# Kernel tuning notes

Hardware: AMD Instinct MI355X
Metric: run time of the kernel (lower is better)

## Reference

```python
import jax, jax.numpy as jnp
import numpy as np

REG_MAX = 16
NUM_CLASSES = 80
STRIDES = (32, 16, 8)
HWS = [(20, 20), (40, 40), (80, 80)]
OFFSET = 0.5


def _conv(x, w, b=None, pad=0):
    out = jax.lax.conv_general_dilated(x, w, (1, 1), [(pad, pad), (pad, pad)],
                                       dimension_numbers=('NCHW', 'OIHW', 'NCHW'))
    if b is not None:
        out = out + b[None, :, None, None]
    return out


def _swish(x):
    return x * jax.nn.sigmoid(x)


def _ese(feat, avg, fc_w, fc_b, conv_w, bn_s, bn_b):
    # ESEAttn: sigmoid-gated 1x1 conv + BN(affine, eval) + swish
    gate = jax.nn.sigmoid(_conv(avg, fc_w, fc_b))
    x = _conv(feat * gate, conv_w)
    return _swish(x * bn_s[None, :, None, None] + bn_b[None, :, None, None])


def _head_scale(feat, ps, proj):
    (cfw, cfb, ccw, cbs, cbb, rfw, rfb, rcw, rbs, rbb, pcw, pcb, prw, prb) = ps
    b, c, h, w = feat.shape
    l = h * w
    avg = jnp.mean(feat, axis=(2, 3), keepdims=True)  # adaptive_avg_pool2d to 1x1
    cls_logit = _conv(_ese(feat, avg, cfw, cfb, ccw, cbs, cbb) + feat, pcw, pcb, pad=1)
    cls_score = jax.nn.sigmoid(cls_logit).reshape(b, NUM_CLASSES, l)
    reg = _conv(_ese(feat, avg, rfw, rfb, rcw, rbs, rbb), prw, prb, pad=1)
    reg = reg.reshape(b, 4, REG_MAX + 1, l).transpose(0, 2, 1, 3)  # [b, reg_max+1, 4, l]
    reg = jax.nn.softmax(reg, axis=1)
    reg_dist = jnp.einsum('r,brfl->bfl', proj, reg)  # DFL integral (proj_conv)
    return cls_score, reg_dist


def _anchors():
    pts, st = [], []
    for (h, w), s in zip(HWS, STRIDES):
        sx = jnp.arange(w, dtype=jnp.float32) + OFFSET
        sy = jnp.arange(h, dtype=jnp.float32) + OFFSET
        yy, xx = jnp.meshgrid(sy, sx, indexing='ij')
        pts.append(jnp.stack([xx, yy], -1).reshape(-1, 2))
        st.append(jnp.full((h * w, 1), s, dtype=jnp.float32))
    return jnp.concatenate(pts, 0), jnp.concatenate(st, 0)


def setup_inputs() -> dict:
    key = jax.random.key(0)
    chans = [1024, 512, 256]
    B = 16
    keys = iter(jax.random.split(key, 128))
    inp = {}
    for i, (c, (h, w)) in enumerate(zip(chans, HWS)):
        s = 1.0 / np.sqrt(c)
        inp[f'feat{i}'] = jax.random.normal(next(keys), (B, c, h, w), jnp.float32)
        for br in ('cls', 'reg'):
            inp[f'p{i}_{br}_fc_w'] = jax.random.normal(next(keys), (c, c, 1, 1), jnp.float32) * 0.001
            inp[f'p{i}_{br}_fc_b'] = jnp.zeros((c,), jnp.float32)
            inp[f'p{i}_{br}_conv_w'] = jax.random.normal(next(keys), (c, c, 1, 1), jnp.float32) * s
            inp[f'p{i}_{br}_bn_s'] = 1.0 + 0.1 * jax.random.normal(next(keys), (c,), jnp.float32)
            inp[f'p{i}_{br}_bn_b'] = 0.1 * jax.random.normal(next(keys), (c,), jnp.float32)
        inp[f'p{i}_cls_pred_w'] = jax.random.normal(next(keys), (NUM_CLASSES, c, 3, 3), jnp.float32) * s * 0.1
        inp[f'p{i}_cls_pred_b'] = jnp.full((NUM_CLASSES,), -4.595, jnp.float32)  # bias_init_with_prob(0.01)
        inp[f'p{i}_reg_pred_w'] = jax.random.normal(next(keys), (4 * (REG_MAX + 1), c, 3, 3), jnp.float32) * s * 0.1
        inp[f'p{i}_reg_pred_b'] = jnp.ones((4 * (REG_MAX + 1),), jnp.float32)
    return inp


def reference(feat0, feat1, feat2,
              p0_cls_fc_w, p0_cls_fc_b, p0_cls_conv_w, p0_cls_bn_s, p0_cls_bn_b,
              p0_reg_fc_w, p0_reg_fc_b, p0_reg_conv_w, p0_reg_bn_s, p0_reg_bn_b,
              p0_cls_pred_w, p0_cls_pred_b, p0_reg_pred_w, p0_reg_pred_b,
              p1_cls_fc_w, p1_cls_fc_b, p1_cls_conv_w, p1_cls_bn_s, p1_cls_bn_b,
              p1_reg_fc_w, p1_reg_fc_b, p1_reg_conv_w, p1_reg_bn_s, p1_reg_bn_b,
              p1_cls_pred_w, p1_cls_pred_b, p1_reg_pred_w, p1_reg_pred_b,
              p2_cls_fc_w, p2_cls_fc_b, p2_cls_conv_w, p2_cls_bn_s, p2_cls_bn_b,
              p2_reg_fc_w, p2_reg_fc_b, p2_reg_conv_w, p2_reg_bn_s, p2_reg_bn_b,
              p2_cls_pred_w, p2_cls_pred_b, p2_reg_pred_w, p2_reg_pred_b):
    proj = jnp.arange(REG_MAX + 1, dtype=jnp.float32)  # linspace(0, reg_max, reg_max+1)
    feats = [feat0, feat1, feat2]
    params = [
        (p0_cls_fc_w, p0_cls_fc_b, p0_cls_conv_w, p0_cls_bn_s, p0_cls_bn_b,
         p0_reg_fc_w, p0_reg_fc_b, p0_reg_conv_w, p0_reg_bn_s, p0_reg_bn_b,
         p0_cls_pred_w, p0_cls_pred_b, p0_reg_pred_w, p0_reg_pred_b),
        (p1_cls_fc_w, p1_cls_fc_b, p1_cls_conv_w, p1_cls_bn_s, p1_cls_bn_b,
         p1_reg_fc_w, p1_reg_fc_b, p1_reg_conv_w, p1_reg_bn_s, p1_reg_bn_b,
         p1_cls_pred_w, p1_cls_pred_b, p1_reg_pred_w, p1_reg_pred_b),
        (p2_cls_fc_w, p2_cls_fc_b, p2_cls_conv_w, p2_cls_bn_s, p2_cls_bn_b,
         p2_reg_fc_w, p2_reg_fc_b, p2_reg_conv_w, p2_reg_bn_s, p2_reg_bn_b,
         p2_cls_pred_w, p2_cls_pred_b, p2_reg_pred_w, p2_reg_pred_b),
    ]
    cls_list, reg_list = [], []
    for feat, ps in zip(feats, params):
        c, r = _head_scale(feat, ps, proj)
        cls_list.append(c)
        reg_list.append(r)
    cls_score = jnp.concatenate(cls_list, -1)   # [b, 80, 8400]
    reg_dist = jnp.concatenate(reg_list, -1)    # [b, 4, 8400]
    anchor_points, stride_tensor = _anchors()
    return cls_score, reg_dist, anchor_points, stride_tensor
```

## Files before the change

kernel.cpp:

```cpp
#include <hip/hip_runtime.h>
#include <hip/hip_bf16.h>


typedef short s8v __attribute__((ext_vector_type(8)));
typedef float f4v __attribute__((ext_vector_type(4)));

#define OUT_REG   10752000ull
#define OUT_ANC   11289600ull
#define OUT_STR   11306400ull

__device__ __forceinline__ unsigned short f2bf(float f) {
    unsigned u = __float_as_uint(f);
    u += 0x7fffu + ((u >> 16) & 1u);
    return (unsigned short)(u >> 16);
}
__device__ __forceinline__ float bf2f(unsigned short h) {
    return __uint_as_float(((unsigned)h) << 16);
}
__device__ __forceinline__ void gl16(const void* g, void* l) {
    __builtin_amdgcn_global_load_lds((const __attribute__((address_space(1))) void*)g,
                                     (__attribute__((address_space(3))) void*)l, 16, 0, 0);
}

__global__ void k_fill0(uint4* __restrict__ p, long n16) {
    uint4 z = make_uint4(0u, 0u, 0u, 0u);
    for (long i = blockIdx.x * 256 + threadIdx.x; i < n16; i += (long)gridDim.x * 256)
        p[i] = z;
}

__global__ void k_avgpool(const float* __restrict__ feat, float* __restrict__ avg, int L) {
    int bc = blockIdx.x;
    const float* p = feat + (size_t)bc * L;
    float s = 0.f;
    for (int i = threadIdx.x; i < L; i += blockDim.x) s += p[i];
#pragma unroll
    for (int off = 32; off > 0; off >>= 1) s += __shfl_down(s, off, 64);
    __shared__ float wsum[4];
    int wid = threadIdx.x >> 6, lane = threadIdx.x & 63;
    if (lane == 0) wsum[wid] = s;
    __syncthreads();
    if (threadIdx.x == 0)
        avg[bc] = (wsum[0] + wsum[1] + wsum[2] + wsum[3]) / (float)L;
}

__global__ void k_gate(const float* __restrict__ avg,
                       const float* __restrict__ fcw_c, const float* __restrict__ fcb_c,
                       const float* __restrict__ fcw_r, const float* __restrict__ fcb_r,
                       float* __restrict__ gc, float* __restrict__ gr, int C) {
    const float* fcw = blockIdx.y ? fcw_r : fcw_c;
    const float* fcb = blockIdx.y ? fcb_r : fcb_c;
    float* g = blockIdx.y ? gr : gc;
    int col = threadIdx.x & 15;
    int b   = threadIdx.x >> 4;
    int co  = blockIdx.x * 16 + col;
    const float* wrow = fcw + (size_t)co * C;
    const float* arow = avg + (size_t)b * C;
    float s = fcb[co];
    for (int ci = 0; ci < C; ++ci) s += wrow[ci] * arow[ci];
    g[(size_t)b * C + co] = 1.f / (1.f + expf(-s));
}

__global__ void k_wcvt(const float* __restrict__ w, unsigned short* __restrict__ o, int n4) {
    for (int i = blockIdx.x * 256 + threadIdx.x; i < n4; i += gridDim.x * 256) {
        float4 v = ((const float4*)w)[i];
        ushort4 u = make_ushort4(f2bf(v.x), f2bf(v.y), f2bf(v.z), f2bf(v.w));
        ((ushort4*)o)[i] = u;
    }
}

__global__ void k_wt3(const float* __restrict__ src, unsigned short* __restrict__ dst,
                      int C, int M, int n) {
    int nineC = 9 * C;
    for (int idx = blockIdx.x * 256 + threadIdx.x; idx < n; idx += gridDim.x * 256) {
        int co = idx / nineC, r = idx - co * nineC;
        int tap = r / C, ci = r - tap * C;
        unsigned short v = 0;
        if (co < M)
            v = f2bf(src[(size_t)co * C * 9 + (size_t)ci * 9 + tap]);
        dst[idx] = v;
    }
}

template<bool WR>
__global__ __launch_bounds__(256) void k_prep(const float* __restrict__ feat,
                                              const float* __restrict__ gate,
                                              unsigned short* __restrict__ Bbuf,
                                              unsigned short* __restrict__ Xpad,
                                              int C, int L, int W, int Wp, int Hp) {
    int b = blockIdx.z, ci0 = blockIdx.y * 32, p0 = blockIdx.x * 32;
    __shared__ float S[32][33];
    int t = threadIdx.x;
    {
        int cil = t >> 3, pl4 = (t & 7) * 4;
        int p = p0 + pl4;
        const float* src = feat + ((size_t)(b * C + ci0 + cil)) * L + p;
        float4 v = make_float4(0.f, 0.f, 0.f, 0.f);
        if (p + 3 < L) v = *(const float4*)src;
        else {
            if (p < L)     v.x = src[0];
            if (p + 1 < L) v.y = src[1];
            if (p + 2 < L) v.z = src[2];
            if (p + 3 < L) v.w = src[3];
        }
        S[cil][pl4] = v.x; S[cil][pl4 + 1] = v.y;
        S[cil][pl4 + 2] = v.z; S[cil][pl4 + 3] = v.w;
    }
    __syncthreads();
    int pl = t >> 3, ci4 = (t & 7) * 4;
    int p = p0 + pl;
    if (p < L) {
        float4 g = *(const float4*)(gate + (size_t)b * C + ci0 + ci4);
        float f0 = S[ci4][pl], f1 = S[ci4 + 1][pl], f2 = S[ci4 + 2][pl], f3 = S[ci4 + 3][pl];
        ushort4 ug = make_ushort4(f2bf(f0 * g.x), f2bf(f1 * g.y), f2bf(f2 * g.z), f2bf(f3 * g.w));
        *(ushort4*)(Bbuf + ((size_t)b * L + p) * C + ci0 + ci4) = ug;
        if (WR) {
            int y = p / W, x = p - y * W;
            ushort4 uf = make_ushort4(f2bf(f0), f2bf(f1), f2bf(f2), f2bf(f3));
            *(ushort4*)(Xpad + (((size_t)b * Hp + 1 + y) * Wp + 1 + x) * C + ci0 + ci4) = uf;
        }
    }
}

template<bool RES>
__global__ __launch_bounds__(256) void k_ese(const unsigned short* __restrict__ Ab,
                                             const unsigned short* __restrict__ Wm,
                                             const float* __restrict__ bns,
                                             const float* __restrict__ bnb,
                                             unsigned short* __restrict__ Xpad,
                                             int C, int L, int W, int Wp, int Hp) {
    int b = blockIdx.z;
    int p0 = blockIdx.x * 128, co0 = blockIdx.y * 128;
    __shared__ unsigned short As[128 * 32];
    __shared__ unsigned short Bs[128 * 32];
    int t = threadIdx.x, lane = t & 63, w = t >> 6;
    int l15 = lane & 15, kg = lane >> 4;
    int mbase = (w >> 1) * 64, nbase = (w & 1) * 64;
    int swb = ((kg ^ (l15 & 3) ^ ((l15 >> 2) & 3)) << 4);
    int slog = (t & 3) ^ ((t >> 2) & 3) ^ ((t >> 4) & 3);
    int r = t >> 2;
    size_t aRow = ((size_t)b * L + p0 + r) * C + 8 * slog;
    size_t bRow = ((size_t)(co0 + r)) * C + 8 * slog;
    size_t rstep = (size_t)64 * C;

    f4v acc[4][4];
#pragma unroll
    for (int i = 0; i < 4; ++i)
#pragma unroll
        for (int j = 0; j < 4; ++j) acc[i][j] = {0.f, 0.f, 0.f, 0.f};

    for (int k0 = 0; k0 < C; k0 += 32) {
        gl16(Ab + aRow + k0,         (char*)As + t * 16);
        gl16(Ab + aRow + rstep + k0, (char*)As + 4096 + t * 16);
        gl16(Wm + bRow + k0,         (char*)Bs + t * 16);
        gl16(Wm + bRow + rstep + k0, (char*)Bs + 4096 + t * 16);
        __syncthreads();
        s8v af[4], bv[4];
#pragma unroll
        for (int i = 0; i < 4; ++i)
            af[i] = *(const s8v*)((const char*)As + ((mbase + i * 16 + l15) << 6) + swb);
#pragma unroll
        for (int i = 0; i < 4; ++i)
            bv[i] = *(const s8v*)((const char*)Bs + ((nbase + i * 16 + l15) << 6) + swb);
#pragma unroll
        for (int mf = 0; mf < 4; ++mf)
#pragma unroll
            for (int nf = 0; nf < 4; ++nf)
                acc[mf][nf] = __builtin_amdgcn_mfma_f32_16x16x32_bf16(af[mf], bv[nf], acc[mf][nf], 0, 0, 0);
        __syncthreads();
    }

    float sv[4], bvv[4];
#pragma unroll
    for (int nf = 0; nf < 4; ++nf) {
        int co = co0 + nbase + nf * 16 + l15;
        sv[nf] = bns[co]; bvv[nf] = bnb[co];
    }
    int cobase = co0 + nbase + l15;
#pragma unroll
    for (int mf = 0; mf < 4; ++mf) {
#pragma unroll
        for (int rg = 0; rg < 4; ++rg) {
            int p = p0 + mbase + mf * 16 + 4 * kg + rg;
            if (p < L) {
                int y = p / W, x = p - y * W;
                size_t rowb = (((size_t)b * Hp + 1 + y) * Wp + 1 + x) * C + cobase;
#pragma unroll
                for (int nf = 0; nf < 4; ++nf) {
                    float v = acc[mf][nf][rg] * sv[nf] + bvv[nf];
                    v = v / (1.f + __expf(-v));
                    unsigned short* dst = Xpad + rowb + nf * 16;
                    if (RES) v += bf2f(*dst);
                    *dst = f2bf(v);
                }
            }
        }
    }
}

template<bool ATOMIC>
__global__ __launch_bounds__(256, 2) void k_conv3(const unsigned short* __restrict__ Xpad,
                                                  const unsigned short* __restrict__ Wt,
                                                  float* __restrict__ part,
                                                  int C, int KC, int H, int W,
                                                  int Hp, int Wp, int M) {
    int b = blockIdx.y;
    int L = H * W;
    int t = threadIdx.x, lane = t & 63, w = t >> 6;
    int l15 = lane & 15, kg = lane >> 4;
    int pw0 = blockIdx.x * 256 + w * 64;
    int nineC = 9 * C;
    int ciS = blockIdx.z * KC;

    int  pn[4];
    long basen[4];
#pragma unroll
    for (int nf = 0; nf < 4; ++nf) {
        int p = pw0 + nf * 16 + l15;
        pn[nf] = p;
        int pc = p < L ? p : L - 1;
        int y = pc / W, x = pc - y * W;
        basen[nf] = (((long)b * Hp + 1 + y) * Wp + 1 + x) * C + ciS + 8 * kg;
    }
    long wb[5];
#pragma unroll
    for (int mf = 0; mf < 5; ++mf)
        wb[mf] = (long)(mf * 16 + l15) * nineC + ciS + 8 * kg;

    f4v acc[5][4];
#pragma unroll
    for (int i = 0; i < 5; ++i)
#pragma unroll
        for (int j = 0; j < 4; ++j) acc[i][j] = {0.f, 0.f, 0.f, 0.f};

    for (int c0 = 0; c0 < KC; c0 += 32) {
#pragma unroll
        for (int ky = 0; ky < 3; ++ky) {
#pragma unroll
            for (int kx = 0; kx < 3; ++kx) {
                int tap = ky * 3 + kx;
                long toff = ((long)(ky - 1) * Wp + (kx - 1)) * C + c0;
                s8v a[5], bv[4];
#pragma unroll
                for (int mf = 0; mf < 5; ++mf)
                    a[mf] = *(const s8v*)(Wt + wb[mf] + tap * C + c0);
#pragma unroll
                for (int nf = 0; nf < 4; ++nf)
                    bv[nf] = *(const s8v*)(Xpad + basen[nf] + toff);
#pragma unroll
                for (int mf = 0; mf < 5; ++mf)
#pragma unroll
                    for (int nf = 0; nf < 4; ++nf)
                        acc[mf][nf] = __builtin_amdgcn_mfma_f32_16x16x32_bf16(a[mf], bv[nf], acc[mf][nf], 0, 0, 0);
            }
        }
    }

#pragma unroll
    for (int mf = 0; mf < 5; ++mf) {
#pragma unroll
        for (int rg = 0; rg < 4; ++rg) {
            int co = mf * 16 + 4 * kg + rg;
            if (co < M) {
                float* op = part + ((long)b * M + co) * L;
#pragma unroll
                for (int nf = 0; nf < 4; ++nf) {
                    if (pn[nf] < L) {
                        float v = acc[mf][nf][rg];
                        if (ATOMIC) unsafeAtomicAdd(op + pn[nf], v);
                        else        op[pn[nf]] = v;
                    }
                }
            }
        }
    }
}

__global__ void k_actcls(const float* __restrict__ part, const float* __restrict__ bias,
                         float* __restrict__ out, int L, int off) {
    long n4 = (long)16 * 80 * L / 4;
    long Lq = L / 4;
    for (long i = blockIdx.x * 256 + threadIdx.x; i < n4; i += (long)gridDim.x * 256) {
        float4 v = ((const float4*)part)[i];
        int p4 = (int)(i % Lq) * 4;
        int co = (int)((i / Lq) % 80);
        int b  = (int)(i / (Lq * 80));
        float bb = bias[co];
        v.x = 1.f / (1.f + __expf(-(v.x + bb)));
        v.y = 1.f / (1.f + __expf(-(v.y + bb)));
        v.z = 1.f / (1.f + __expf(-(v.z + bb)));
        v.w = 1.f / (1.f + __expf(-(v.w + bb)));
        *(float4*)(out + (long)b * 672000 + (long)co * 8400 + off + p4) = v;
    }
}

__global__ void k_dfl(const float* __restrict__ logits, const float* __restrict__ pb,
                      float* __restrict__ out, int L, int scale_off) {
    int idx = blockIdx.x * 256 + threadIdx.x;
    int total = 16 * 4 * L;
    if (idx >= total) return;
    int p = idx % L, r = idx / L, f = r & 3, b = r >> 2;
    const float* lp = logits + ((size_t)b * 68 + f * 17) * L + p;
    float v[17], mx = -1e30f;
#pragma unroll
    for (int j = 0; j < 17; ++j) {
        v[j] = lp[(size_t)j * L] + pb[f * 17 + j];
        mx = fmaxf(mx, v[j]);
    }
    float s = 0.f, d = 0.f;
#pragma unroll
    for (int j = 0; j < 17; ++j) {
        float e = __expf(v[j] - mx);
        s += e; d += e * (float)j;
    }
    out[OUT_REG + ((size_t)b * 4 + f) * 8400 + scale_off + p] = d / s;
}

__global__ void k_anchors(float* __restrict__ out) {
    int idx = blockIdx.x * 256 + threadIdx.x;
    if (idx >= 8400) return;
    int w, base; float s;
    if (idx < 400)       { w = 20; s = 32.f; base = 0; }
    else if (idx < 2000) { w = 40; s = 16.f; base = 400; }
    else                 { w = 80; s = 8.f;  base = 2000; }
    int r = idx - base;
    int row = r / w, col = r % w;
    out[OUT_ANC + (size_t)idx * 2]     = (float)col + 0.5f;
    out[OUT_ANC + (size_t)idx * 2 + 1] = (float)row + 0.5f;
    out[OUT_STR + idx] = s;
}

extern "C" void kernel_launch(void* const* d_in, const int* in_sizes, int n_in,
                              void* d_out, int out_size, void* d_ws, size_t ws_size,
                              hipStream_t stream) {
    const int B = 16;
    static const int Cs[3] = {1024, 512, 256};
    static const int Hs[3] = {20, 40, 80};
    static const int offs[3] = {0, 400, 2000};
    static const int NSs[3] = {16, 4, 1};

    char* ws = (char*)d_ws;
    unsigned short* Bbuf = (unsigned short*)ws;
    float*          part = (float*)ws;
    unsigned short* Xpad = (unsigned short*)(ws + 52428800);
    unsigned short* Wb   = (unsigned short*)(ws + 107511808);
    unsigned short* Wt   = (unsigned short*)(ws + 109608960);
    float* avg = (float*)(ws + 111083520);
    float* gc  = (float*)(ws + 111149056);
    float* gr  = (float*)(ws + 111214592);
    float* out = (float*)d_out;

    for (int i = 0; i < 3; ++i) {
        const int base = i * 15;
        const float* feat = (const float*)d_in[base + 0];
        const float* cfw  = (const float*)d_in[base + 1];
        const float* cfb  = (const float*)d_in[base + 2];
        const float* ccw  = (const float*)d_in[base + 3];
        const float* cbs  = (const float*)d_in[base + 4];
        const float* cbb  = (const float*)d_in[base + 5];
        const float* rfw  = (const float*)d_in[base + 6];
        const float* rfb  = (const float*)d_in[base + 7];
        const float* rcw  = (const float*)d_in[base + 8];
        const float* rbs  = (const float*)d_in[base + 9];
        const float* rbb  = (const float*)d_in[base + 10];
        const float* pcw  = (const float*)d_in[base + 11];
        const float* pcb  = (const float*)d_in[base + 12];
        const float* prw  = (const float*)d_in[base + 13];
        const float* prb  = (const float*)d_in[base + 14];

        int C = Cs[i], H = Hs[i], W = H, L = H * W, Hp = H + 2, Wp = W + 2;
        int NS = NSs[i], KC = C / NS;

        long n16 = (long)B * Hp * Wp * C * 2 / 16;
        k_fill0<<<2048, 256, 0, stream>>>((uint4*)Xpad, n16);
        k_avgpool<<<B * C, 256, 0, stream>>>(feat, avg, L);
        k_gate<<<dim3(C / 16, 2), 256, 0, stream>>>(avg, cfw, cfb, rfw, rfb, gc, gr, C);

        dim3 gprep((L + 31) / 32, C / 32, B);
        dim3 gese((L + 127) / 128, C / 128, B);
        dim3 gcv((L + 255) / 256, B, NS);

        k_wcvt<<<1024, 256, 0, stream>>>(ccw, Wb, C * C / 4);
        k_prep<true><<<gprep, 256, 0, stream>>>(feat, gc, Bbuf, Xpad, C, L, W, Wp, Hp);
        k_ese<true><<<gese, 256, 0, stream>>>(Bbuf, Wb, cbs, cbb, Xpad, C, L, W, Wp, Hp);
        k_wt3<<<(80 * 9 * C + 255) / 256, 256, 0, stream>>>(pcw, Wt, C, 80, 80 * 9 * C);
        if (NS > 1) {
            k_fill0<<<1024, 256, 0, stream>>>((uint4*)part, (long)80 * L * 4);
            k_conv3<true><<<gcv, 256, 0, stream>>>(Xpad, Wt, part, C, KC, H, W, Hp, Wp, 80);
        } else {
            k_conv3<false><<<gcv, 256, 0, stream>>>(Xpad, Wt, part, C, KC, H, W, Hp, Wp, 80);
        }
        k_actcls<<<1024, 256, 0, stream>>>(part, pcb, out, L, offs[i]);

        k_wcvt<<<1024, 256, 0, stream>>>(rcw, Wb, C * C / 4);
        k_prep<false><<<gprep, 256, 0, stream>>>(feat, gr, Bbuf, Xpad, C, L, W, Wp, Hp);
        k_ese<false><<<gese, 256, 0, stream>>>(Bbuf, Wb, rbs, rbb, Xpad, C, L, W, Wp, Hp);
        k_wt3<<<(80 * 9 * C + 255) / 256, 256, 0, stream>>>(prw, Wt, C, 68, 80 * 9 * C);
        if (NS > 1) {
            k_fill0<<<1024, 256, 0, stream>>>((uint4*)part, (long)68 * L * 4);
            k_conv3<true><<<gcv, 256, 0, stream>>>(Xpad, Wt, part, C, KC, H, W, Hp, Wp, 68);
        } else {
            k_conv3<false><<<gcv, 256, 0, stream>>>(Xpad, Wt, part, C, KC, H, W, Hp, Wp, 68);
        }
        k_dfl<<<(B * 4 * L + 255) / 256, 256, 0, stream>>>(part, prb, out, L, offs[i]);
    }
    k_anchors<<<33, 256, 0, stream>>>(out);
}
```

Before: 1.641 ms.

## Stage 3x3 conv input tiles in LDS with row reuse and halo-only zeroing

```diff
diff --git a/kernel.cpp b/kernel.cpp
--- a/kernel.cpp
+++ b/kernel.cpp
@@ -26,6 +26,31 @@
     uint4 z = make_uint4(0u, 0u, 0u, 0u);
     for (long i = blockIdx.x * 256 + threadIdx.x; i < n16; i += (long)gridDim.x * 256)
         p[i] = z;
+}
+
+__global__ void k_fillhalo(unsigned short* __restrict__ Xpad, int Hp, int Wp, int C) {
+    int rowC = Wp * C;
+    long T8 = (long)(2 * rowC + 2 * (Hp - 2) * C) / 8;
+    long n8 = 16 * T8;
+    uint4 z = make_uint4(0u, 0u, 0u, 0u);
+    for (long i = blockIdx.x * 256 + threadIdx.x; i < n8; i += (long)gridDim.x * 256) {
+        int b = (int)(i / T8);
+        long e = (i % T8) * 8;
+        long addr;
+        if (e < rowC) {
+            addr = ((long)b * Hp) * rowC + e;
+        } else if (e < 2L * rowC) {
+            addr = ((long)b * Hp + Hp - 1) * rowC + (e - rowC);
+        } else {
+            long e2 = e - 2L * rowC;
+            int y = 1 + (int)(e2 / (2 * C));
+            int r = (int)(e2 % (2 * C));
+            int col = (r < C) ? 0 : (Wp - 1);
+            int ci = (r < C) ? r : r - C;
+            addr = (((long)b * Hp + y) * Wp + col) * (long)C + ci;
+        }
+        *(uint4*)(Xpad + addr) = z;
+    }
 }
 
 __global__ void k_avgpool(const float* __restrict__ feat, float* __restrict__ avg, int L) {
@@ -197,79 +222,108 @@
     }
 }
 
-template<bool ATOMIC>
-__global__ __launch_bounds__(256, 2) void k_conv3(const unsigned short* __restrict__ Xpad,
-                                                  const unsigned short* __restrict__ Wt,
-                                                  float* __restrict__ part,
-                                                  int C, int KC, int H, int W,
-                                                  int Hp, int Wp, int M) {
-    int b = blockIdx.y;
-    int L = H * W;
-    int t = threadIdx.x, lane = t & 63, w = t >> 6;
-    int l15 = lane & 15, kg = lane >> 4;
-    int pw0 = blockIdx.x * 256 + w * 64;
-    int nineC = 9 * C;
-    int ciS = blockIdx.z * KC;
-
-    int  pn[4];
-    long basen[4];
-#pragma unroll
-    for (int nf = 0; nf < 4; ++nf) {
-        int p = pw0 + nf * 16 + l15;
-        pn[nf] = p;
-        int pc = p < L ? p : L - 1;
-        int y = pc / W, x = pc - y * W;
-        basen[nf] = (((long)b * Hp + 1 + y) * Wp + 1 + x) * C + ciS + 8 * kg;
-    }
-    long wb[5];
-#pragma unroll
-    for (int mf = 0; mf < 5; ++mf)
-        wb[mf] = (long)(mf * 16 + l15) * nineC + ciS + 8 * kg;
-
-    f4v acc[5][4];
-#pragma unroll
-    for (int i = 0; i < 5; ++i)
-#pragma unroll
-        for (int j = 0; j < 4; ++j) acc[i][j] = {0.f, 0.f, 0.f, 0.f};
+template<int WT>
+__global__ __launch_bounds__(320, 2) void k_conv3t(const unsigned short* __restrict__ Xpad,
+                                                   const unsigned short* __restrict__ Wt,
+                                                   float* __restrict__ part,
+                                                   int C, int KC, int Hp, int Wp, int M) {
+    constexpr int BR    = 80 / WT;
+    constexpr int R     = 400 / WT;
+    constexpr int LROWS = R + 2;
+    constexpr int LCOLS = WT + 2;
+    constexpr int UNITS = LROWS * LCOLS;
+    constexpr int TOT   = UNITS * 4;
+    constexpr int NEWL  = (BR < 3) ? BR : 3;
+    __shared__ char lds[UNITS * 64];
+
+    const int b  = blockIdx.y;
+    const int bx = blockIdx.x;
+    const int L  = WT * WT;
+    const int t  = threadIdx.x, lane = t & 63, w = t >> 6;
+    const int l15 = lane & 15, kg = lane >> 4;
+    const int ciS = blockIdx.z * KC;
+    const int nineC = 9 * C;
+    const int y0 = bx * R;
+
+    const int lp0  = w * 16 + l15;
+    const int ly00 = lp0 / WT;
+    const int lx0  = lp0 % WT;
+
+    long wbase[5];
+#pragma unroll
+    for (int m = 0; m < 5; ++m)
+        wbase[m] = (long)(m * 16 + l15) * nineC + ciS + 8 * kg;
+
+    f4v acc[5][5];
+#pragma unroll
+    for (int m = 0; m < 5; ++m)
+#pragma unroll
+        for (int i = 0; i < 5; ++i) acc[m][i] = {0.f, 0.f, 0.f, 0.f};
+
+    const char* ldsw = lds + (kg << 4);
 
     for (int c0 = 0; c0 < KC; c0 += 32) {
-#pragma unroll
-        for (int ky = 0; ky < 3; ++ky) {
-#pragma unroll
-            for (int kx = 0; kx < 3; ++kx) {
-                int tap = ky * 3 + kx;
-                long toff = ((long)(ky - 1) * Wp + (kx - 1)) * C + c0;
-                s8v a[5], bv[4];
-#pragma unroll
-                for (int mf = 0; mf < 5; ++mf)
-                    a[mf] = *(const s8v*)(Wt + wb[mf] + tap * C + c0);
-#pragma unroll
-                for (int nf = 0; nf < 4; ++nf)
-                    bv[nf] = *(const s8v*)(Xpad + basen[nf] + toff);
-#pragma unroll
-                for (int mf = 0; mf < 5; ++mf)
-#pragma unroll
-                    for (int nf = 0; nf < 4; ++nf)
-                        acc[mf][nf] = __builtin_amdgcn_mfma_f32_16x16x32_bf16(a[mf], bv[nf], acc[mf][nf], 0, 0, 0);
+        __syncthreads();
+#pragma unroll
+        for (int it = 0; it < (TOT + 319) / 320; ++it) {
+            int c = it * 320 + t;
+            if (c < TOT) {
+                int q = c >> 2, slot = c & 3;
+                int row = q / LCOLS, col = q % LCOLS;
+                int srcslot = slot ^ (q & 3) ^ ((q >> 2) & 3);
+                const unsigned short* src = Xpad +
+                    (((size_t)b * Hp + y0 + row) * Wp + col) * C + ciS + c0 + srcslot * 8;
+                gl16(src, lds + (it * 320 + (t & ~63)) * 16);
             }
         }
-    }
-
-#pragma unroll
-    for (int mf = 0; mf < 5; ++mf) {
+        __syncthreads();
+
+#pragma unroll
+        for (int kx = 0; kx < 3; ++kx) {
+            s8v a[3][5];
+#pragma unroll
+            for (int ky = 0; ky < 3; ++ky)
+#pragma unroll
+                for (int m = 0; m < 5; ++m)
+                    a[ky][m] = *(const s8v*)(Wt + wbase[m] + (ky * 3 + kx) * C + c0);
+
+            s8v ring[4];
+#define LOADB(roff)                                                              \
+            {                                                                    \
+                int u_ = (ly00 + (roff)) * LCOLS + lx0 + kx;                     \
+                ring[(roff) & 3] = *(const s8v*)(ldsw + (u_ << 6) +              \
+                                   (((u_ & 3) ^ ((u_ >> 2) & 3)) << 4));         \
+            }
+            LOADB(0); LOADB(1); LOADB(2);
+#pragma unroll
+            for (int i = 0; i < 5; ++i) {
+                if (i > 0) {
+#pragma unroll
+                    for (int d = 3 - NEWL; d < 3; ++d) LOADB(BR * i + d);
+                }
+#pragma unroll
+                for (int ky = 0; ky < 3; ++ky) {
+                    s8v bf = ring[(BR * i + ky) & 3];
+#pragma unroll
+                    for (int m = 0; m < 5; ++m)
+                        acc[m][i] = __builtin_amdgcn_mfma_f32_16x16x32_bf16(a[ky][m], bf, acc[m][i], 0, 0, 0);
+                }
+            }
+#undef LOADB
+        }
+    }
+
+    const int pbase = bx * 400 + w * 16 + l15;
+#pragma unroll
+    for (int m = 0; m < 5; ++m) {
 #pragma unroll
         for (int rg = 0; rg < 4; ++rg) {
-            int co = mf * 16 + 4 * kg + rg;
+            int co = m * 16 + 4 * kg + rg;
             if (co < M) {
-                float* op = part + ((long)b * M + co) * L;
-#pragma unroll
-                for (int nf = 0; nf < 4; ++nf) {
-                    if (pn[nf] < L) {
-                        float v = acc[mf][nf][rg];
-                        if (ATOMIC) unsafeAtomicAdd(op + pn[nf], v);
-                        else        op[pn[nf]] = v;
-                    }
-                }
+                float* op = part + ((long)b * M + co) * L + pbase;
+#pragma unroll
+                for (int i = 0; i < 5; ++i)
+                    unsafeAtomicAdd(op + i * 80, acc[m][i][rg]);
             }
         }
     }
@@ -336,7 +390,7 @@
     static const int Cs[3] = {1024, 512, 256};
     static const int Hs[3] = {20, 40, 80};
     static const int offs[3] = {0, 400, 2000};
-    static const int NSs[3] = {16, 4, 1};
+    static const int NSs[3] = {32, 8, 2};
 
     char* ws = (char*)d_ws;
     unsigned short* Bbuf = (unsigned short*)ws;
@@ -370,37 +424,32 @@
         int C = Cs[i], H = Hs[i], W = H, L = H * W, Hp = H + 2, Wp = W + 2;
         int NS = NSs[i], KC = C / NS;
 
-        long n16 = (long)B * Hp * Wp * C * 2 / 16;
-        k_fill0<<<2048, 256, 0, stream>>>((uint4*)Xpad, n16);
+        k_fillhalo<<<512, 256, 0, stream>>>(Xpad, Hp, Wp, C);
         k_avgpool<<<B * C, 256, 0, stream>>>(feat, avg, L);
         k_gate<<<dim3(C / 16, 2), 256, 0, stream>>>(avg, cfw, cfb, rfw, rfb, gc, gr, C);
 
         dim3 gprep((L + 31) / 32, C / 32, B);
         dim3 gese((L + 127) / 128, C / 128, B);
-        dim3 gcv((L + 255) / 256, B, NS);
+        dim3 gcv(L / 400, B, NS);
 
         k_wcvt<<<1024, 256, 0, stream>>>(ccw, Wb, C * C / 4);
         k_prep<true><<<gprep, 256, 0, stream>>>(feat, gc, Bbuf, Xpad, C, L, W, Wp, Hp);
         k_ese<true><<<gese, 256, 0, stream>>>(Bbuf, Wb, cbs, cbb, Xpad, C, L, W, Wp, Hp);
         k_wt3<<<(80 * 9 * C + 255) / 256, 256, 0, stream>>>(pcw, Wt, C, 80, 80 * 9 * C);
-        if (NS > 1) {
-            k_fill0<<<1024, 256, 0, stream>>>((uint4*)part, (long)80 * L * 4);
-            k_conv3<true><<<gcv, 256, 0, stream>>>(Xpad, Wt, part, C, KC, H, W, Hp, Wp, 80);
-        } else {
-            k_conv3<false><<<gcv, 256, 0, stream>>>(Xpad, Wt, part, C, KC, H, W, Hp, Wp, 80);
-        }
+        k_fill0<<<1024, 256, 0, stream>>>((uint4*)part, (long)B * 80 * L / 4);
+        if (i == 0)      k_conv3t<20><<<gcv, 320, 0, stream>>>(Xpad, Wt, part, C, KC, Hp, Wp, 80);
+        else if (i == 1) k_conv3t<40><<<gcv, 320, 0, stream>>>(Xpad, Wt, part, C, KC, Hp, Wp, 80);
+        else             k_conv3t<80><<<gcv, 320, 0, stream>>>(Xpad, Wt, part, C, KC, Hp, Wp, 80);
         k_actcls<<<1024, 256, 0, stream>>>(part, pcb, out, L, offs[i]);
 
         k_wcvt<<<1024, 256, 0, stream>>>(rcw, Wb, C * C / 4);
         k_prep<false><<<gprep, 256, 0, stream>>>(feat, gr, Bbuf, Xpad, C, L, W, Wp, Hp);
         k_ese<false><<<gese, 256, 0, stream>>>(Bbuf, Wb, rbs, rbb, Xpad, C, L, W, Wp, Hp);
         k_wt3<<<(80 * 9 * C + 255) / 256, 256, 0, stream>>>(prw, Wt, C, 68, 80 * 9 * C);
-        if (NS > 1) {
-            k_fill0<<<1024, 256, 0, stream>>>((uint4*)part, (long)68 * L * 4);
-            k_conv3<true><<<gcv, 256, 0, stream>>>(Xpad, Wt, part, C, KC, H, W, Hp, Wp, 68);
-        } else {
-            k_conv3<false><<<gcv, 256, 0, stream>>>(Xpad, Wt, part, C, KC, H, W, Hp, Wp, 68);
-        }
+        k_fill0<<<1024, 256, 0, stream>>>((uint4*)part, (long)B * 68 * L / 4);
+        if (i == 0)      k_conv3t<20><<<gcv, 320, 0, stream>>>(Xpad, Wt, part, C, KC, Hp, Wp, 68);
+        else if (i == 1) k_conv3t<40><<<gcv, 320, 0, stream>>>(Xpad, Wt, part, C, KC, Hp, Wp, 68);
+        else             k_conv3t<80><<<gcv, 320, 0, stream>>>(Xpad, Wt, part, C, KC, Hp, Wp, 68);
         k_dfl<<<(B * 4 * L + 255) / 256, 256, 0, stream>>>(part, prb, out, L, offs[i]);
     }
     k_anchors<<<33, 256, 0, stream>>>(out);
```

Measured after the change: 1.561 ms. 1.05x faster.
